# Kernel tuning notes

Measured on AMD Instinct MI355X. Metric: run time of the kernel, lower is better.

Reference implementation:

```python
import jax, jax.numpy as jnp
import numpy as np

N_NODES = 100000
N_EDGES = 3200000
N_FEAT = 128
N_GRAPHS = 1024
N_CLASSES = 10
K = 30  # global_sort_pool k


def setup_inputs() -> dict:
    key = jax.random.key(0)
    ks = jax.random.split(key, 20)
    p = lambda k, shape: jax.random.normal(k, shape, jnp.float32) * 0.1
    return {
        "x": jax.random.normal(ks[0], (N_NODES, N_FEAT), jnp.float32),
        "w1": p(ks[1], (N_FEAT, 32)), "b1": p(ks[2], (32,)),
        "w2": p(ks[3], (32, 32)),     "b2": p(ks[4], (32,)),
        "w3": p(ks[5], (32, 32)),     "b3": p(ks[6], (32,)),
        "w4": p(ks[7], (32, 1)),      "b4": p(ks[8], (1,)),
        "conv5_w": p(ks[9], (16, 1, 97)),  "conv5_b": p(ks[10], (16,)),
        "conv6_w": p(ks[11], (32, 16, 5)), "conv6_b": p(ks[12], (32,)),
        "fc1_w": p(ks[13], (352, 128)),    "fc1_b": p(ks[14], (128,)),
        "fc2_w": p(ks[15], (128, N_CLASSES)), "fc2_b": p(ks[16], (N_CLASSES,)),
        "edge_src": jax.random.randint(ks[17], (N_EDGES,), 0, N_NODES),
        "edge_dst": jax.random.randint(ks[18], (N_EDGES,), 0, N_NODES),
        "batch": jnp.sort(jax.random.randint(ks[19], (N_NODES,), 0, N_GRAPHS)),
        "num_graphs": N_GRAPHS,
    }


def _gcn_forward(x, w1, b1, w2, b2, w3, b3, w4, b4,
                 conv5_w, conv5_b, conv6_w, conv6_b,
                 fc1_w, fc1_b, fc2_w, fc2_b,
                 edge_src, edge_dst, batch, num_graphs):
    n = x.shape[0]
    # remove_self_loops: mask self-loop edges to weight 0 (shapes stay static)
    ew = (edge_src != edge_dst).astype(x.dtype)
    # gcn_norm with added self-loops (weight 1): deg includes self-loop
    deg = jax.ops.segment_sum(ew, edge_dst, num_segments=n) + 1.0
    dis = jax.lax.rsqrt(deg)                       # deg^{-1/2}
    enorm = dis[edge_src] * dis[edge_dst] * ew     # [E]
    snorm = (dis * dis)[:, None]                   # self-loop norm [n,1]

    def gcn_conv(h, W, b):
        h = h @ W                                   # [n, out]
        agg = jax.ops.segment_sum(h[edge_src] * enorm[:, None], edge_dst,
                                  num_segments=n) + h * snorm
        return agg + b

    x1 = jnp.tanh(gcn_conv(x,  w1, b1))   # [n,32]
    x2 = jnp.tanh(gcn_conv(x1, w2, b2))   # [n,32]
    x3 = jnp.tanh(gcn_conv(x2, w3, b3))   # [n,32]
    x4 = jnp.tanh(gcn_conv(x3, w4, b4))   # [n,1]
    xc = jnp.concatenate([x1, x2, x3, x4], axis=-1)  # [n,97]

    # global_sort_pool(k=K): per-graph sort by last channel, descending
    key_last = xc[:, -1]
    order = jnp.lexsort((-key_last, batch))          # primary: batch, secondary: desc key
    bs = batch[order]                                # sorted graph ids
    counts = jax.ops.segment_sum(jnp.ones_like(batch, jnp.int32), batch,
                                 num_segments=num_graphs)
    starts = jnp.cumsum(counts) - counts             # exclusive prefix sum
    rank = jnp.arange(n) - starts[bs]                # rank within own graph
    r = jnp.where(rank < K, rank, K)                 # overflow -> dummy slot K
    pooled = jnp.zeros((num_graphs, K + 1, 97), xc.dtype)
    pooled = pooled.at[bs, r].set(xc[order])
    pooled = pooled[:, :K, :].reshape(num_graphs, 1, K * 97)  # [B,1,2910]

    # Conv1d(1,16,97,97) + relu
    h = jax.lax.conv_general_dilated(pooled, conv5_w, (97,), 'VALID',
                                     dimension_numbers=('NCH', 'OIH', 'NCH'))
    h = jax.nn.relu(h + conv5_b[None, :, None])      # [B,16,30]
    # MaxPool1d(2,2)
    h = jax.lax.reduce_window(h, -jnp.inf, jax.lax.max,
                              (1, 1, 2), (1, 1, 2), 'VALID')  # [B,16,15]
    # Conv1d(16,32,5,1) + relu
    h = jax.lax.conv_general_dilated(h, conv6_w, (1,), 'VALID',
                                     dimension_numbers=('NCH', 'OIH', 'NCH'))
    h = jax.nn.relu(h + conv6_b[None, :, None])      # [B,32,11]
    h = h.reshape(num_graphs, -1)                    # [B,352]

    h = jax.nn.relu(h @ fc1_w + fc1_b)               # [B,128]; dropout = identity (eval)
    return jax.nn.log_softmax(h @ fc2_w + fc2_b, axis=-1)  # [B,num_classes]


def reference(x, w1, b1, w2, b2, w3, b3, w4, b4,
              conv5_w, conv5_b, conv6_w, conv6_b,
              fc1_w, fc1_b, fc2_w, fc2_b,
              edge_src, edge_dst, batch, num_graphs):
    return _gcn_forward(x, w1, b1, w2, b2, w3, b3, w4, b4,
                        conv5_w, conv5_b, conv6_w, conv6_b,
                        fc1_w, fc1_b, fc2_w, fc2_b,
                        edge_src, edge_dst, batch, num_graphs)
```

## Files before the change

### kernel.cpp

```cpp
#include <hip/hip_runtime.h>
#include <hip/hip_bf16.h>

#define N_NODES 100000
#define N_EDGES 3200000
#define NGRAPH 1024
#define KTOP 30
#define PELEM (NGRAPH * KTOP * 97)

#define NBKT 782
#define NTILE 391
#define TILE 8192
#define BKT_CAP 4736

typedef __hip_bfloat16 bf16;
typedef float vfloat4 __attribute__((ext_vector_type(4)));

__device__ __forceinline__ float u2f(unsigned short h) {
    return __uint_as_float(((unsigned int)h) << 16);
}
__device__ __forceinline__ float LD(const void* p, int i, int bf) {
    if (bf) return u2f(((const unsigned short*)p)[i]);
    return ((const float*)p)[i];
}

__global__ void k_detect(const void* w1, int* flag) {
    if (threadIdx.x == 0 && blockIdx.x == 0) {
        const unsigned short* u = (const unsigned short*)w1;
        int plausible = 0;
        for (int i = 0; i < 64; i++) {
            float a = fabsf(u2f(u[2 * i]));
            if (a == 0.f || (a >= 9.765625e-4f && a <= 2.0f)) plausible++;
        }
        *flag = (plausible >= 40) ? 1 : 0;
    }
}

__global__ void k_icur(int* __restrict__ cur) {
    int i = blockIdx.x * 256 + threadIdx.x;
    if (i < NBKT) cur[i] = i * BKT_CAP;
}

__global__ __launch_bounds__(256) void k_scat(const int* __restrict__ src,
                                              const int* __restrict__ dst,
                                              int* __restrict__ cur,
                                              int* __restrict__ ebuf) {
    __shared__ int pk[TILE];
    __shared__ unsigned short bk[TILE];
    __shared__ int h[NBKT];
    __shared__ int base[NBKT];
    int tid = threadIdx.x;
    int ebase = blockIdx.x * TILE;
    for (int i = tid; i < NBKT; i += 256) h[i] = 0;
    __syncthreads();
    for (int i = tid; i < TILE; i += 256) {
        int e = ebase + i;
        int bkt = 0xFFFF;
        if (e < N_EDGES) {
            int s = __builtin_nontemporal_load(src + e);
            int d = __builtin_nontemporal_load(dst + e);
            if (s != d) {
                bkt = d >> 7;
                pk[i] = ((d & 127) << 17) | s;
                atomicAdd(&h[bkt], 1);
            }
        }
        bk[i] = (unsigned short)bkt;
    }
    __syncthreads();
    for (int i = tid; i < NBKT; i += 256) {
        int c = h[i];
        base[i] = c ? atomicAdd(&cur[i], c) : 0;
    }
    __syncthreads();
    for (int i = tid; i < NBKT; i += 256) h[i] = 0;
    __syncthreads();
    for (int i = tid; i < TILE; i += 256) {
        int bkt = bk[i];
        if (bkt != 0xFFFF) {
            int p = base[bkt] + atomicAdd(&h[bkt], 1);
            if (p < (bkt + 1) * BKT_CAP) ebuf[p] = pk[i];
        }
    }
}

__global__ __launch_bounds__(256) void k_bcsr(const int* __restrict__ ebuf,
                                              const int* __restrict__ cur,
                                              int* __restrict__ rs,
                                              int* __restrict__ re,
                                              float* __restrict__ dis,
                                              int* __restrict__ csr) {
    __shared__ int dloc[128];
    __shared__ int sc[128];
    int b = blockIdx.x;
    int node0 = b << 7;
    int nn = N_NODES - node0; if (nn > 128) nn = 128;
    int tid = threadIdx.x;
    if (tid < 128) dloc[tid] = 0;
    __syncthreads();
    int s = b * BKT_CAP;
    int cnt = cur[b] - s; if (cnt > BKT_CAP) cnt = BKT_CAP;
    int e = s + cnt;
    for (int i = s + tid; i < e; i += 256)
        atomicAdd(&dloc[ebuf[i] >> 17], 1);
    __syncthreads();
    if (tid < 128) sc[tid] = dloc[tid];
    __syncthreads();
    for (int off = 1; off < 128; off <<= 1) {
        int t = (tid >= off && tid < 128) ? sc[tid - off] : 0;
        __syncthreads();
        if (tid < 128) sc[tid] += t;
        __syncthreads();
    }
    if (tid < nn) {
        int st = s + sc[tid] - dloc[tid];
        rs[node0 + tid] = st;
        re[node0 + tid] = st + dloc[tid];
        dis[node0 + tid] = rsqrtf((float)dloc[tid] + 1.0f);
    }
    __syncthreads();
    if (tid < 128) dloc[tid] = s + sc[tid] - dloc[tid];
    __syncthreads();
    for (int i = s + tid; i < e; i += 256) {
        int pv = ebuf[i];
        int pos = atomicAdd(&dloc[pv >> 17], 1);
        csr[pos] = pv & 0x1FFFF;
    }
}

__global__ void k_gstart(const int* __restrict__ batch, int* __restrict__ gstart) {
    int g = blockIdx.x * 256 + threadIdx.x;
    if (g > NGRAPH) return;
    int lo = 0, hi = N_NODES;
    while (lo < hi) {
        int mid = (lo + hi) >> 1;
        if (batch[mid] < g) lo = mid + 1; else hi = mid;
    }
    gstart[g] = lo;
}

__global__ __launch_bounds__(256) void k_mm1(const void* __restrict__ x,
                                             const void* __restrict__ w,
                                             const int* __restrict__ flagp,
                                             const float* __restrict__ dis,
                                             float* __restrict__ ts) {
    __shared__ float Wl[128 * 32];
    __shared__ float Xs[32][128];
    int bf = *flagp;
    int tid = threadIdx.x;
    int nbase = blockIdx.x * 32;
    if (bf) {
        const ushort4* wv = (const ushort4*)w;
        for (int idx = tid; idx < 1024; idx += 256) {
            ushort4 h = wv[idx];
            int p = idx * 4;
            Wl[p] = u2f(h.x); Wl[p + 1] = u2f(h.y); Wl[p + 2] = u2f(h.z); Wl[p + 3] = u2f(h.w);
        }
        const ushort4* xv = (const ushort4*)x;
        for (int idx = tid; idx < 1024; idx += 256) {
            int nd = idx >> 5, q = idx & 31;
            ushort4 h = xv[(size_t)(nbase + nd) * 32 + q];
            float* d = &Xs[nd][q * 4];
            d[0] = u2f(h.x); d[1] = u2f(h.y); d[2] = u2f(h.z); d[3] = u2f(h.w);
        }
    } else {
        const float* wf = (const float*)w;
        for (int idx = tid; idx < 4096; idx += 256) Wl[idx] = wf[idx];
        const float* xf = (const float*)x;
        for (int idx = tid; idx < 4096; idx += 256)
            Xs[idx >> 7][idx & 127] = xf[(size_t)nbase * 128 + idx];
    }
    __syncthreads();
    int grp = tid >> 5, col = tid & 31;
    for (int rep = 0; rep < 4; rep++) {
        int sub = grp + 8 * rep;
        int node = nbase + sub;
        float acc = 0.f;
#pragma unroll 8
        for (int k = 0; k < 128; k++) acc += Xs[sub][k] * Wl[k * 32 + col];
        ts[node * 32 + col] = dis[node] * acc;
    }
}

__global__ __launch_bounds__(256) void k_mm32(const float* __restrict__ xin,
                                              const void* __restrict__ w,
                                              const int* __restrict__ flagp,
                                              const float* __restrict__ dis,
                                              float* __restrict__ ts) {
    __shared__ float Wl[32 * 32];
    __shared__ float Xs[32][32];
    int bf = *flagp;
    int tid = threadIdx.x;
    int nbase = blockIdx.x * 32;
    if (bf) {
        const ushort4* wv = (const ushort4*)w;
        for (int idx = tid; idx < 256; idx += 256) {
            ushort4 h = wv[idx];
            int p = idx * 4;
            Wl[p] = u2f(h.x); Wl[p + 1] = u2f(h.y); Wl[p + 2] = u2f(h.z); Wl[p + 3] = u2f(h.w);
        }
    } else {
        const float* wf = (const float*)w;
        for (int idx = tid; idx < 1024; idx += 256) Wl[idx] = wf[idx];
    }
    {
        const float4* xv = (const float4*)xin;
        int nd = tid >> 3, q = tid & 7;
        float4 v = xv[(size_t)(nbase + nd) * 8 + q];
        float* d = &Xs[nd][q * 4];
        d[0] = v.x; d[1] = v.y; d[2] = v.z; d[3] = v.w;
    }
    __syncthreads();
    int grp = tid >> 5, col = tid & 31;
    for (int rep = 0; rep < 4; rep++) {
        int sub = grp + 8 * rep;
        int node = nbase + sub;
        float acc = 0.f;
#pragma unroll
        for (int k = 0; k < 32; k++) acc += Xs[sub][k] * Wl[k * 32 + col];
        ts[node * 32 + col] = dis[node] * acc;
    }
}

__global__ __launch_bounds__(256) void k_mm_out1(const float* __restrict__ xin,
                                                 const void* __restrict__ w4,
                                                 const int* __restrict__ flagp,
                                                 const float* __restrict__ dis,
                                                 float* __restrict__ ts4) {
    int node = blockIdx.x * 8 + (threadIdx.x >> 5);
    int lane = threadIdx.x & 31;
    if (node >= N_NODES) return;
    int bf = *flagp;
    float v = xin[node * 32 + lane] * LD(w4, lane, bf);
    for (int off = 16; off; off >>= 1) v += __shfl_down(v, off, 32);
    if (lane == 0) ts4[node] = dis[node] * v;
}

__global__ __launch_bounds__(256) void k_agg32(const float4* __restrict__ ts,
                                               const int* __restrict__ rs,
                                               const int* __restrict__ re,
                                               const int* __restrict__ csr,
                                               const float* __restrict__ dis,
                                               const void* __restrict__ b,
                                               const int* __restrict__ flagp,
                                               float4* __restrict__ out) {
    int node = blockIdx.x * 4 + (threadIdx.x >> 6);
    int lane = threadIdx.x & 63;
    int q   = lane & 7;
    int grp = lane >> 3;
    int bf = *flagp;
    int s = rs[node], e = re[node];
    float4 a0 = make_float4(0.f, 0.f, 0.f, 0.f);
    float4 a1 = a0, a2 = a0, a3 = a0;
    int i = s + grp;
    for (; i + 24 < e; i += 32) {
        int v0 = csr[i], v1 = csr[i + 8], v2 = csr[i + 16], v3 = csr[i + 24];
        float4 m0 = ts[v0 * 8 + q];
        float4 m1 = ts[v1 * 8 + q];
        float4 m2 = ts[v2 * 8 + q];
        float4 m3 = ts[v3 * 8 + q];
        a0.x += m0.x; a0.y += m0.y; a0.z += m0.z; a0.w += m0.w;
        a1.x += m1.x; a1.y += m1.y; a1.z += m1.z; a1.w += m1.w;
        a2.x += m2.x; a2.y += m2.y; a2.z += m2.z; a2.w += m2.w;
        a3.x += m3.x; a3.y += m3.y; a3.z += m3.z; a3.w += m3.w;
    }
    for (; i < e; i += 8) {
        float4 m = ts[csr[i] * 8 + q];
        a0.x += m.x; a0.y += m.y; a0.z += m.z; a0.w += m.w;
    }
    float4 acc;
    acc.x = (a0.x + a1.x) + (a2.x + a3.x);
    acc.y = (a0.y + a1.y) + (a2.y + a3.y);
    acc.z = (a0.z + a1.z) + (a2.z + a3.z);
    acc.w = (a0.w + a1.w) + (a2.w + a3.w);
#pragma unroll
    for (int off = 8; off < 64; off <<= 1) {
        acc.x += __shfl_xor(acc.x, off);
        acc.y += __shfl_xor(acc.y, off);
        acc.z += __shfl_xor(acc.z, off);
        acc.w += __shfl_xor(acc.w, off);
    }
    if (grp == 0) {
        float4 self = ts[node * 8 + q];
        float d = dis[node];
        vfloat4 r;
        r.x = tanhf(d * (acc.x + self.x) + LD(b, q * 4 + 0, bf));
        r.y = tanhf(d * (acc.y + self.y) + LD(b, q * 4 + 1, bf));
        r.z = tanhf(d * (acc.z + self.z) + LD(b, q * 4 + 2, bf));
        r.w = tanhf(d * (acc.w + self.w) + LD(b, q * 4 + 3, bf));
        __builtin_nontemporal_store(r, (vfloat4*)&out[node * 8 + q]);
    }
}

__global__ __launch_bounds__(256) void k_agg1(const float* __restrict__ ts4,
                                              const int* __restrict__ rs,
                                              const int* __restrict__ re,
                                              const int* __restrict__ csr,
                                              const float* __restrict__ dis,
                                              const void* __restrict__ b4,
                                              const int* __restrict__ flagp,
                                              float* __restrict__ x4) {
    int node = blockIdx.x * 16 + (threadIdx.x >> 4);
    int lane = threadIdx.x & 15;
    int s = rs[node], e = re[node];
    float acc = 0.f;
    for (int i = s + lane; i < e; i += 16) acc += ts4[csr[i]];
#pragma unroll
    for (int off = 1; off < 16; off <<= 1) acc += __shfl_xor(acc, off);
    if (lane == 0) {
        int bf = *flagp;
        x4[node] = tanhf(dis[node] * (acc + ts4[node]) + LD(b4, 0, bf));
    }
}

__global__ __launch_bounds__(256) void k_rank(const int* __restrict__ batch,
                                              const int* __restrict__ gstart,
                                              const float* __restrict__ x4,
                                              int* __restrict__ sel) {
    int i = blockIdx.x * 256 + threadIdx.x;
    if (i >= N_NODES) return;
    int g = batch[i];
    int s = gstart[g], e = gstart[g + 1];
    float ki = x4[i];
    int rank = 0;
    for (int j = s; j < e; j++) {
        float kj = x4[j];
        rank += (kj > ki) || (kj == ki && j < i);
    }
    if (rank < KTOP) sel[g * KTOP + rank] = i;
}

__global__ __launch_bounds__(256) void k_pool(const float* __restrict__ x1,
                                              const float* __restrict__ x2,
                                              const float* __restrict__ x3,
                                              const float* __restrict__ x4,
                                              const int* __restrict__ sel,
                                              float* __restrict__ P) {
    int idx = blockIdx.x * 256 + threadIdx.x;
    if (idx >= PELEM) return;
    int g = idx / (KTOP * 97);
    int r = idx - g * (KTOP * 97);
    int p = r / 97;
    int f = r - p * 97;
    int v = sel[g * KTOP + p];
    float val = 0.f;
    if (v >= 0) {
        if (f < 32)      val = x1[v * 32 + f];
        else if (f < 64) val = x2[v * 32 + f - 32];
        else if (f < 96) val = x3[v * 32 + f - 64];
        else             val = x4[v];
    }
    P[idx] = val;
}

__global__ __launch_bounds__(256) void k_head(
    const float* __restrict__ Pg,
    const void* __restrict__ w5, const void* __restrict__ b5,
    const void* __restrict__ w6, const void* __restrict__ b6,
    const void* __restrict__ f1w, const void* __restrict__ f1b,
    const void* __restrict__ f2w, const void* __restrict__ f2b,
    const int* __restrict__ flagp, void* __restrict__ out) {
    __shared__ float P[KTOP * 97];
    __shared__ float W5[16 * 97];
    __shared__ float W6[32 * 16 * 5];
    __shared__ float H5[16][30];
    __shared__ float M[16][15];
    __shared__ float H6[352];
    __shared__ float Rp[256];
    __shared__ float R1[128];
    __shared__ float L[10];
    __shared__ float mls;
    int g = blockIdx.x;
    int tid = threadIdx.x;
    int bf = *flagp;

    for (int i = tid; i < KTOP * 97; i += 256) P[i] = Pg[g * (KTOP * 97) + i];
    if (bf) {
        const ushort4* w5v = (const ushort4*)w5;
        for (int i = tid; i < 388; i += 256) {
            ushort4 h = w5v[i];
            int p = i * 4;
            W5[p] = u2f(h.x); W5[p + 1] = u2f(h.y); W5[p + 2] = u2f(h.z); W5[p + 3] = u2f(h.w);
        }
        const ushort4* w6v = (const ushort4*)w6;
        for (int i = tid; i < 640; i += 256) {
            ushort4 h = w6v[i];
            int p = i * 4;
            W6[p] = u2f(h.x); W6[p + 1] = u2f(h.y); W6[p + 2] = u2f(h.z); W6[p + 3] = u2f(h.w);
        }
    } else {
        for (int i = tid; i < 16 * 97; i += 256) W5[i] = ((const float*)w5)[i];
        for (int i = tid; i < 2560; i += 256) W6[i] = ((const float*)w6)[i];
    }
    __syncthreads();
    for (int idx = tid; idx < 480; idx += 256) {
        int o = idx / 30, p = idx - o * 30;
        float acc = LD(b5, o, bf);
        const float* pr = &P[p * 97];
        const float* wr = &W5[o * 97];
        for (int f = 0; f < 97; f++) acc += wr[f] * pr[f];
        H5[o][p] = fmaxf(acc, 0.f);
    }
    __syncthreads();
    for (int idx = tid; idx < 240; idx += 256) {
        int o = idx / 15, q = idx - o * 15;
        M[o][q] = fmaxf(H5[o][2 * q], H5[o][2 * q + 1]);
    }
    __syncthreads();
    for (int idx = tid; idx < 352; idx += 256) {
        int oc = idx / 11, tp = idx - oc * 11;
        float acc = LD(b6, oc, bf);
        const float* wr = &W6[oc * 80];
        for (int ic = 0; ic < 16; ic++) {
#pragma unroll
            for (int k = 0; k < 5; k++)
                acc += wr[ic * 5 + k] * M[ic][tp + k];
        }
        H6[idx] = fmaxf(acc, 0.f);
    }
    __syncthreads();
    {
        int half = tid >> 7, col = tid & 127;
        int base = half * 176;
        float a = 0.f;
        for (int i = 0; i < 176; i++) {
            int ii = base + i;
            a += H6[ii] * LD(f1w, ii * 128 + col, bf);
        }
        Rp[tid] = a;
    }
    __syncthreads();
    if (tid < 128) R1[tid] = fmaxf(LD(f1b, tid, bf) + Rp[tid] + Rp[128 + tid], 0.f);
    __syncthreads();
    if (tid < 10) {
        float acc = LD(f2b, tid, bf);
        for (int k = 0; k < 128; k++) acc += R1[k] * LD(f2w, k * 10 + tid, bf);
        L[tid] = acc;
    }
    __syncthreads();
    if (tid == 0) {
        float m = L[0];
        for (int c = 1; c < 10; c++) m = fmaxf(m, L[c]);
        float ssum = 0.f;
        for (int c = 0; c < 10; c++) ssum += expf(L[c] - m);
        mls = m + logf(ssum);
    }
    __syncthreads();
    if (tid < 10) {
        float v = L[tid] - mls;
        if (bf) ((bf16*)out)[g * 10 + tid] = __float2bfloat16(v);
        else    ((float*)out)[g * 10 + tid] = v;
    }
}

extern "C" void kernel_launch(void* const* d_in, const int* in_sizes, int n_in,
                              void* d_out, int out_size, void* d_ws, size_t ws_size,
                              hipStream_t stream) {
    const void* x   = d_in[0];
    const void* w1  = d_in[1];  const void* b1  = d_in[2];
    const void* w2  = d_in[3];  const void* b2  = d_in[4];
    const void* w3  = d_in[5];  const void* b3  = d_in[6];
    const void* w4  = d_in[7];  const void* b4  = d_in[8];
    const void* w5  = d_in[9];  const void* b5  = d_in[10];
    const void* w6  = d_in[11]; const void* b6  = d_in[12];
    const void* f1w = d_in[13]; const void* f1b = d_in[14];
    const void* f2w = d_in[15]; const void* f2b = d_in[16];
    const int* esrc  = (const int*)d_in[17];
    const int* edst  = (const int*)d_in[18];
    const int* batch = (const int*)d_in[19];

    char* w = (char*)d_ws;
    size_t off = 0;
    auto alloc = [&](size_t bytes) {
        void* p = w + off;
        off += (bytes + 255) & ~(size_t)255;
        return p;
    };
    int*   flag   = (int*)  alloc(256);
    int*   rs     = (int*)  alloc((size_t)N_NODES * 4);
    int*   re     = (int*)  alloc((size_t)N_NODES * 4);
    float* dis    = (float*)alloc((size_t)N_NODES * 4);
    int*   csr    = (int*)  alloc((size_t)NBKT * BKT_CAP * 4);
    float* t      = (float*)alloc((size_t)N_NODES * 32 * 4);
    float* x1     = (float*)alloc((size_t)N_NODES * 32 * 4);
    float* x2     = (float*)alloc((size_t)N_NODES * 32 * 4);
    float* x3     = (float*)alloc((size_t)N_NODES * 32 * 4);
    float* x4     = (float*)alloc((size_t)N_NODES * 4);
    int*   gstart = (int*)  alloc((size_t)(NGRAPH + 1) * 4);
    int*   sel    = (int*)  alloc((size_t)NGRAPH * KTOP * 4);
    float* Pg     = (float*)alloc((size_t)PELEM * 4);
    int*   cur    = (int*)  alloc((size_t)NBKT * 4);
    (void)ws_size; (void)n_in; (void)in_sizes; (void)out_size;

    int* ebuf = (int*)t;

    (void)hipMemsetAsync(sel, 0xFF, (size_t)NGRAPH * KTOP * 4, stream);

    int nb   = (N_NODES + 255) / 256;
    int mb32 = N_NODES / 32;
    int ab   = N_NODES / 4;
    int a1b  = N_NODES / 16;
    int pb   = (PELEM + 255) / 256;

    k_detect<<<1, 64, 0, stream>>>(w1, flag);
    k_icur<<<(NBKT + 255) / 256, 256, 0, stream>>>(cur);
    k_scat<<<NTILE, 256, 0, stream>>>(esrc, edst, cur, ebuf);
    k_bcsr<<<NBKT, 256, 0, stream>>>(ebuf, cur, rs, re, dis, csr);
    k_gstart<<<5, 256, 0, stream>>>(batch, gstart);

    k_mm1<<<mb32, 256, 0, stream>>>(x, w1, flag, dis, t);
    k_agg32<<<ab, 256, 0, stream>>>((const float4*)t, rs, re, csr, dis, b1, flag, (float4*)x1);
    k_mm32<<<mb32, 256, 0, stream>>>(x1, w2, flag, dis, t);
    k_agg32<<<ab, 256, 0, stream>>>((const float4*)t, rs, re, csr, dis, b2, flag, (float4*)x2);
    k_mm32<<<mb32, 256, 0, stream>>>(x2, w3, flag, dis, t);
    k_agg32<<<ab, 256, 0, stream>>>((const float4*)t, rs, re, csr, dis, b3, flag, (float4*)x3);
    k_mm_out1<<<(N_NODES + 7) / 8, 256, 0, stream>>>(x3, w4, flag, dis, t);
    k_agg1<<<a1b, 256, 0, stream>>>(t, rs, re, csr, dis, b4, flag, x4);
    k_rank<<<nb, 256, 0, stream>>>(batch, gstart, x4, sel);
    k_pool<<<pb, 256, 0, stream>>>(x1, x2, x3, x4, sel, Pg);
    k_head<<<NGRAPH, 256, 0, stream>>>(Pg, w5, b5, w6, b6,
                                       f1w, f1b, f2w, f2b, flag, (void*)d_out);
}
```

Measured before the change: 597.7 us.

## Fuse next-layer GCN matmul into aggregation kernel epilogue

Removes the separate k_mm32 and k_mm_out1 kernels. Each aggregation block now stages its four tanh-activated rows in shared memory and applies the next layer's weight matrix (32x32, or 32x1 for the last conv), writing the dis-scaled transform directly. This saves three kernel launches and a full re-read of the activations from global memory. In exchange, every aggregation block loads the weight matrix and adds a __syncthreads, and a second transform buffer is used for ping-pong.

```diff
diff --git a/kernel.cpp b/kernel.cpp
--- a/kernel.cpp
+++ b/kernel.cpp
@@ -181,73 +181,40 @@
     }
 }
 
-__global__ __launch_bounds__(256) void k_mm32(const float* __restrict__ xin,
-                                              const void* __restrict__ w,
+template<int OUTF>
+__global__ __launch_bounds__(256) void k_aggf(const float4* __restrict__ ts,
+                                              const int* __restrict__ rs,
+                                              const int* __restrict__ re,
+                                              const int* __restrict__ csr,
+                                              const float* __restrict__ dis,
+                                              const void* __restrict__ b,
+                                              const void* __restrict__ Wn,
                                               const int* __restrict__ flagp,
-                                              const float* __restrict__ dis,
-                                              float* __restrict__ ts) {
-    __shared__ float Wl[32 * 32];
-    __shared__ float Xs[32][32];
+                                              float4* __restrict__ out,
+                                              float* __restrict__ tsn) {
+    __shared__ float Wl[OUTF == 1 ? 32 : 1024];
+    __shared__ float Xrow[4][32];
+    int tid = threadIdx.x;
     int bf = *flagp;
-    int tid = threadIdx.x;
-    int nbase = blockIdx.x * 32;
-    if (bf) {
-        const ushort4* wv = (const ushort4*)w;
-        for (int idx = tid; idx < 256; idx += 256) {
-            ushort4 h = wv[idx];
-            int p = idx * 4;
+    if (OUTF == 32) {
+        if (bf) {
+            ushort4 h = ((const ushort4*)Wn)[tid];
+            int p = tid * 4;
             Wl[p] = u2f(h.x); Wl[p + 1] = u2f(h.y); Wl[p + 2] = u2f(h.z); Wl[p + 3] = u2f(h.w);
+        } else {
+            float4 v = ((const float4*)Wn)[tid];
+            int p = tid * 4;
+            Wl[p] = v.x; Wl[p + 1] = v.y; Wl[p + 2] = v.z; Wl[p + 3] = v.w;
         }
     } else {
-        const float* wf = (const float*)w;
-        for (int idx = tid; idx < 1024; idx += 256) Wl[idx] = wf[idx];
-    }
-    {
-        const float4* xv = (const float4*)xin;
-        int nd = tid >> 3, q = tid & 7;
-        float4 v = xv[(size_t)(nbase + nd) * 8 + q];
-        float* d = &Xs[nd][q * 4];
-        d[0] = v.x; d[1] = v.y; d[2] = v.z; d[3] = v.w;
-    }
-    __syncthreads();
-    int grp = tid >> 5, col = tid & 31;
-    for (int rep = 0; rep < 4; rep++) {
-        int sub = grp + 8 * rep;
-        int node = nbase + sub;
-        float acc = 0.f;
-#pragma unroll
-        for (int k = 0; k < 32; k++) acc += Xs[sub][k] * Wl[k * 32 + col];
-        ts[node * 32 + col] = dis[node] * acc;
-    }
-}
-
-__global__ __launch_bounds__(256) void k_mm_out1(const float* __restrict__ xin,
-                                                 const void* __restrict__ w4,
-                                                 const int* __restrict__ flagp,
-                                                 const float* __restrict__ dis,
-                                                 float* __restrict__ ts4) {
-    int node = blockIdx.x * 8 + (threadIdx.x >> 5);
-    int lane = threadIdx.x & 31;
-    if (node >= N_NODES) return;
-    int bf = *flagp;
-    float v = xin[node * 32 + lane] * LD(w4, lane, bf);
-    for (int off = 16; off; off >>= 1) v += __shfl_down(v, off, 32);
-    if (lane == 0) ts4[node] = dis[node] * v;
-}
-
-__global__ __launch_bounds__(256) void k_agg32(const float4* __restrict__ ts,
-                                               const int* __restrict__ rs,
-                                               const int* __restrict__ re,
-                                               const int* __restrict__ csr,
-                                               const float* __restrict__ dis,
-                                               const void* __restrict__ b,
-                                               const int* __restrict__ flagp,
-                                               float4* __restrict__ out) {
-    int node = blockIdx.x * 4 + (threadIdx.x >> 6);
-    int lane = threadIdx.x & 63;
+        if (tid < 32) Wl[tid] = LD(Wn, tid, bf);
+    }
+
+    int wid = tid >> 6;
+    int node = blockIdx.x * 4 + wid;
+    int lane = tid & 63;
     int q   = lane & 7;
     int grp = lane >> 3;
-    int bf = *flagp;
     int s = rs[node], e = re[node];
     float4 a0 = make_float4(0.f, 0.f, 0.f, 0.f);
     float4 a1 = a0, a2 = a0, a3 = a0;
@@ -288,6 +255,35 @@
         r.z = tanhf(d * (acc.z + self.z) + LD(b, q * 4 + 2, bf));
         r.w = tanhf(d * (acc.w + self.w) + LD(b, q * 4 + 3, bf));
         __builtin_nontemporal_store(r, (vfloat4*)&out[node * 8 + q]);
+        Xrow[wid][q * 4 + 0] = r.x;
+        Xrow[wid][q * 4 + 1] = r.y;
+        Xrow[wid][q * 4 + 2] = r.z;
+        Xrow[wid][q * 4 + 3] = r.w;
+    }
+    __syncthreads();
+    if (OUTF == 32) {
+        int nd = tid >> 6;
+        int col = tid & 31;
+        int kbase = (tid & 32) >> 1;
+        const float* xr = Xrow[nd];
+        float a = 0.f;
+#pragma unroll
+        for (int k2 = 0; k2 < 16; k2++) a += xr[kbase + k2] * Wl[(kbase + k2) * 32 + col];
+        a += __shfl_xor(a, 32);
+        if (!(tid & 32)) {
+            int n2 = blockIdx.x * 4 + nd;
+            tsn[n2 * 32 + col] = dis[n2] * a;
+        }
+    } else {
+        int g8 = tid >> 5;
+        if (g8 < 4) {
+            int n2 = blockIdx.x * 4 + g8;
+            int k = tid & 31;
+            float a = Xrow[g8][k] * Wl[k];
+#pragma unroll
+            for (int off = 16; off; off >>= 1) a += __shfl_xor(a, off);
+            if (k == 0) tsn[n2] = dis[n2] * a;
+        }
     }
 }
 
@@ -481,6 +477,7 @@
     float* dis    = (float*)alloc((size_t)N_NODES * 4);
     int*   csr    = (int*)  alloc((size_t)NBKT * BKT_CAP * 4);
     float* t      = (float*)alloc((size_t)N_NODES * 32 * 4);
+    float* t2     = (float*)alloc((size_t)N_NODES * 32 * 4);
     float* x1     = (float*)alloc((size_t)N_NODES * 32 * 4);
     float* x2     = (float*)alloc((size_t)N_NODES * 32 * 4);
     float* x3     = (float*)alloc((size_t)N_NODES * 32 * 4);
@@ -508,13 +505,10 @@
     k_gstart<<<5, 256, 0, stream>>>(batch, gstart);
 
     k_mm1<<<mb32, 256, 0, stream>>>(x, w1, flag, dis, t);
-    k_agg32<<<ab, 256, 0, stream>>>((const float4*)t, rs, re, csr, dis, b1, flag, (float4*)x1);
-    k_mm32<<<mb32, 256, 0, stream>>>(x1, w2, flag, dis, t);
-    k_agg32<<<ab, 256, 0, stream>>>((const float4*)t, rs, re, csr, dis, b2, flag, (float4*)x2);
-    k_mm32<<<mb32, 256, 0, stream>>>(x2, w3, flag, dis, t);
-    k_agg32<<<ab, 256, 0, stream>>>((const float4*)t, rs, re, csr, dis, b3, flag, (float4*)x3);
-    k_mm_out1<<<(N_NODES + 7) / 8, 256, 0, stream>>>(x3, w4, flag, dis, t);
-    k_agg1<<<a1b, 256, 0, stream>>>(t, rs, re, csr, dis, b4, flag, x4);
+    k_aggf<32><<<ab, 256, 0, stream>>>((const float4*)t,  rs, re, csr, dis, b1, w2, flag, (float4*)x1, t2);
+    k_aggf<32><<<ab, 256, 0, stream>>>((const float4*)t2, rs, re, csr, dis, b2, w3, flag, (float4*)x2, t);
+    k_aggf<1><<<ab, 256, 0, stream>>>((const float4*)t,  rs, re, csr, dis, b3, w4, flag, (float4*)x3, t2);
+    k_agg1<<<a1b, 256, 0, stream>>>(t2, rs, re, csr, dis, b4, flag, x4);
     k_rank<<<nb, 256, 0, stream>>>(batch, gstart, x4, sel);
     k_pool<<<pb, 256, 0, stream>>>(x1, x2, x3, x4, sel, Pg);
     k_head<<<NGRAPH, 256, 0, stream>>>(Pg, w5, b5, w6, b6,
```

Measured after the change: 587.2 us. About the same (-1.8%).
